# Kernel tuning notes

Hardware: AMD Instinct MI355X
Metric: run time of the kernel (lower is better)

Reference implementation:

```python
import jax, jax.numpy as jnp
import numpy as np
from jax.ops import segment_sum

N_NODES = 100000

def setup_inputs() -> dict:
    key = jax.random.key(0)
    k1, k2, k3 = jax.random.split(key, 3)
    x = jax.random.normal(k1, (N_NODES, 128), dtype=jnp.float32)
    edge_weight = jax.random.uniform(k2, (3200000,), dtype=jnp.float32)
    edge_index = jax.random.randint(k3, (2, 3200000), 0, N_NODES, dtype=jnp.int64)
    return {"x": x, "edge_weight": edge_weight, "edge_index": edge_index}

def reference(x, edge_weight, edge_index):
    # GCNConv with weight forced to identity (in==out channels, no bias):
    # lin(x) == x, so the op is gcn_norm + scatter-add aggregation.
    n = x.shape[0]
    # add self loops with fill value 1.0 (improved=False)
    loop_idx = jnp.arange(n, dtype=edge_index.dtype)
    row = jnp.concatenate([edge_index[0], loop_idx])
    col = jnp.concatenate([edge_index[1], loop_idx])
    ew = jnp.concatenate([edge_weight, jnp.ones((n,), dtype=edge_weight.dtype)])
    # symmetric normalization: deg computed at target (col)
    deg = segment_sum(ew, col, num_segments=n)
    dinv = jnp.where(deg > 0, jax.lax.rsqrt(deg), 0.0)
    norm = dinv[row] * ew * dinv[col]
    # message = norm * x[src]; aggregate (sum) at target
    msgs = x[row] * norm[:, None]          # [E+N, d]
    out = segment_sum(msgs, col, num_segments=n)  # [N, d]
    return out
```

## Files before the change

### kernel.cpp

```cpp
#include <hip/hip_runtime.h>
#include <hip/hip_fp16.h>
#include <math.h>

#define FEAT    128
#define PITCH   72
#define CH      6144
#define K_EDGES 12
#define MAXBINS 512

__global__ void zero_meta_kernel(float* __restrict__ deg, int* __restrict__ countg,
                                 int* __restrict__ cursor, int n, int nbins) {
    int i = blockIdx.x * blockDim.x + threadIdx.x;
    if (i < n) { deg[i] = 0.0f; countg[i] = 0; }
    if (i < nbins) cursor[i] = 0;
}

__global__ void conv_xs_kernel(const float* __restrict__ x,
                               const float* __restrict__ deg,
                               __half2* __restrict__ xs, int n4) {
    int i = blockIdx.x * blockDim.x + threadIdx.x;
    if (i >= n4) return;
    float s = rsqrtf(1.0f + deg[i >> 5]);
    float4 v = ((const float4*)x)[i];
    xs[2 * i]     = __floats2half2_rn(s * v.x, s * v.y);
    xs[2 * i + 1] = __floats2half2_rn(s * v.z, s * v.w);
}

__global__ __launch_bounds__(512) void p1_partition_kernel(
        const int* __restrict__ row,
        const int* __restrict__ col,
        const float* __restrict__ ew,
        int* __restrict__ bin_cursor,
        unsigned long long* __restrict__ binned,
        int E, int NBINS, int cap) {
    __shared__ unsigned long long stage[CH];
    __shared__ int hist[MAXBINS];
    __shared__ int lofs[MAXBINS];
    __shared__ int lcnt[MAXBINS];
    __shared__ int gbase[MAXBINS];
    __shared__ int scanbuf[MAXBINS];
    int tid = threadIdx.x;
    if (tid < MAXBINS) { hist[tid] = 0; lcnt[tid] = 0; }
    __syncthreads();

    int start = blockIdx.x * CH;
    int end   = start + CH; if (end > E) end = E;
    int total = end - start;

    unsigned long long ed[K_EDGES];
    int ebin[K_EDGES];
    #pragma unroll
    for (int k = 0; k < K_EDGES; k++) {
        int e = start + (k << 9) + tid;
        if (e < end) {
            int c = col[e];
            unsigned short wh = __half_as_ushort(__float2half_rn(ew[e]));
            ed[k] = ((unsigned long long)wh << 48)
                  | ((unsigned long long)((unsigned)row[e] & 0xFFFFFFu) << 24)
                  | (unsigned)(c & 0xFFFFFFu);
            ebin[k] = c >> 8;
            atomicAdd(&hist[ebin[k]], 1);
        } else {
            ebin[k] = -1;
        }
    }
    __syncthreads();

    int h = (tid < NBINS) ? hist[tid] : 0;
    scanbuf[tid] = h;
    __syncthreads();
    #pragma unroll
    for (int off = 1; off < MAXBINS; off <<= 1) {
        int t = (tid >= off) ? scanbuf[tid - off] : 0;
        __syncthreads();
        scanbuf[tid] += t;
        __syncthreads();
    }
    lofs[tid] = scanbuf[tid] - h;
    __syncthreads();

    #pragma unroll
    for (int k = 0; k < K_EDGES; k++) {
        if (ebin[k] >= 0) {
            int pos = lofs[ebin[k]] + atomicAdd(&lcnt[ebin[k]], 1);
            stage[pos] = ed[k];
        }
    }
    if (tid < NBINS)
        gbase[tid] = hist[tid] ? atomicAdd(&bin_cursor[tid], hist[tid]) : 0;
    __syncthreads();

    for (int i = tid; i < total; i += 512) {
        unsigned long long e = stage[i];
        int bin = (int)((e >> 8) & 0xFFFFu);
        int pos = gbase[bin] + (i - lofs[bin]);
        if (pos < cap) binned[(size_t)bin * cap + pos] = e;
    }
}

__global__ __launch_bounds__(256) void p2_build_kernel(
        const unsigned long long* __restrict__ binned,
        const int* __restrict__ bin_cursor,
        unsigned long long* __restrict__ bucket,
        float* __restrict__ deg,
        int* __restrict__ countg,
        int N, int cap) {
    __shared__ float degp[256];
    __shared__ int   cnt[256];
    int tid = threadIdx.x;
    degp[tid] = 0.0f;
    cnt[tid]  = 0;
    __syncthreads();

    int b = blockIdx.x >> 1, hf = blockIdx.x & 1;
    int nE = bin_cursor[b]; if (nE > cap) nE = cap;
    int half = nE >> 1;
    int lo = hf ? half : 0;
    int hi = hf ? nE : half;
    const unsigned long long* src = binned + (size_t)b * cap;
    int nodeBase = b << 8;

    for (int i = lo + tid; i < hi; i += 256) {
        unsigned long long p = src[i];
        int cl = (int)(p & 255u);
        int r  = (int)((p >> 24) & 0xFFFFFFu);
        float w = __half2float(__ushort_as_half((unsigned short)(p >> 48)));
        int slot = atomicAdd(&cnt[cl], 1);
        atomicAdd(&degp[cl], w);
        if (slot < PITCH) {
            int pos = hf ? (PITCH - 1 - slot) : slot;
            bucket[(size_t)(nodeBase + cl) * PITCH + pos] =
                ((unsigned long long)__float_as_uint(w) << 32) | (unsigned)r;
        }
    }
    __syncthreads();

    int node = nodeBase + tid;
    if (node < N) {
        int c2 = cnt[tid]; if (c2 > PITCH) c2 = PITCH;
        if (c2) atomicAdd(&countg[node], hf ? (c2 << 16) : c2);
        float d = degp[tid];
        if (d != 0.0f) atomicAdd(&deg[node], d);
    }
}

__global__ __launch_bounds__(256) void gather_xs_kernel(
        const __half2* __restrict__ xs,
        const float* __restrict__ deg,
        const int* __restrict__ countg,
        const unsigned long long* __restrict__ bucket,
        float* __restrict__ out, int n) {
    __shared__ unsigned long long eb[4][64];
    int wid  = threadIdx.x >> 6;
    int node = blockIdx.x * 4 + wid;
    int lane = threadIdx.x & 63;
    if (node >= n) return;

    float di = rsqrtf(1.0f + deg[node]);
    int c = countg[node];
    int cnt0 = c & 0xFFFF, cnt1 = (c >> 16) & 0xFFFF;
    int cnt = cnt0 + cnt1; if (cnt > PITCH) cnt = PITCH;

    const unsigned long long* b = bucket + (size_t)node * PITCH;
    int idx = (lane < cnt0) ? lane : (PITCH - 1 - (lane - cnt0));
    unsigned long long e0 = (lane < cnt) ? b[idx] : 0ULL;
    eb[wid][lane] = e0;

    unsigned xbase = ((unsigned)node << 6) | (unsigned)lane;
    float2 xv = __half22float2(xs[xbase]);
    float2 a0 = xv;
    float2 a1 = {0.f, 0.f}, a2 = {0.f, 0.f}, a3 = {0.f, 0.f};

    int m = cnt < 64 ? cnt : 64;
    int j = 0;
    for (; j + 8 <= m; j += 8) {
        unsigned long long p0 = eb[wid][j + 0];
        unsigned long long p1 = eb[wid][j + 1];
        unsigned long long p2 = eb[wid][j + 2];
        unsigned long long p3 = eb[wid][j + 3];
        unsigned long long p4 = eb[wid][j + 4];
        unsigned long long p5 = eb[wid][j + 5];
        unsigned long long p6 = eb[wid][j + 6];
        unsigned long long p7 = eb[wid][j + 7];
        unsigned r0 = (unsigned)p0, r1 = (unsigned)p1, r2 = (unsigned)p2, r3 = (unsigned)p3;
        unsigned r4 = (unsigned)p4, r5 = (unsigned)p5, r6 = (unsigned)p6, r7 = (unsigned)p7;
        float w0 = __uint_as_float((unsigned)(p0 >> 32));
        float w1 = __uint_as_float((unsigned)(p1 >> 32));
        float w2 = __uint_as_float((unsigned)(p2 >> 32));
        float w3 = __uint_as_float((unsigned)(p3 >> 32));
        float w4 = __uint_as_float((unsigned)(p4 >> 32));
        float w5 = __uint_as_float((unsigned)(p5 >> 32));
        float w6 = __uint_as_float((unsigned)(p6 >> 32));
        float w7 = __uint_as_float((unsigned)(p7 >> 32));
        float2 v0 = __half22float2(xs[(r0 << 6) | lane]);
        float2 v1 = __half22float2(xs[(r1 << 6) | lane]);
        float2 v2 = __half22float2(xs[(r2 << 6) | lane]);
        float2 v3 = __half22float2(xs[(r3 << 6) | lane]);
        float2 v4 = __half22float2(xs[(r4 << 6) | lane]);
        float2 v5 = __half22float2(xs[(r5 << 6) | lane]);
        float2 v6 = __half22float2(xs[(r6 << 6) | lane]);
        float2 v7 = __half22float2(xs[(r7 << 6) | lane]);
        a0.x = fmaf(w0, v0.x, a0.x);  a0.y = fmaf(w0, v0.y, a0.y);
        a1.x = fmaf(w1, v1.x, a1.x);  a1.y = fmaf(w1, v1.y, a1.y);
        a2.x = fmaf(w2, v2.x, a2.x);  a2.y = fmaf(w2, v2.y, a2.y);
        a3.x = fmaf(w3, v3.x, a3.x);  a3.y = fmaf(w3, v3.y, a3.y);
        a0.x = fmaf(w4, v4.x, a0.x);  a0.y = fmaf(w4, v4.y, a0.y);
        a1.x = fmaf(w5, v5.x, a1.x);  a1.y = fmaf(w5, v5.y, a1.y);
        a2.x = fmaf(w6, v6.x, a2.x);  a2.y = fmaf(w6, v6.y, a2.y);
        a3.x = fmaf(w7, v7.x, a3.x);  a3.y = fmaf(w7, v7.y, a3.y);
    }
    for (; j + 4 <= m; j += 4) {
        unsigned long long p0 = eb[wid][j + 0];
        unsigned long long p1 = eb[wid][j + 1];
        unsigned long long p2 = eb[wid][j + 2];
        unsigned long long p3 = eb[wid][j + 3];
        unsigned r0 = (unsigned)p0, r1 = (unsigned)p1, r2 = (unsigned)p2, r3 = (unsigned)p3;
        float w0 = __uint_as_float((unsigned)(p0 >> 32));
        float w1 = __uint_as_float((unsigned)(p1 >> 32));
        float w2 = __uint_as_float((unsigned)(p2 >> 32));
        float w3 = __uint_as_float((unsigned)(p3 >> 32));
        float2 v0 = __half22float2(xs[(r0 << 6) | lane]);
        float2 v1 = __half22float2(xs[(r1 << 6) | lane]);
        float2 v2 = __half22float2(xs[(r2 << 6) | lane]);
        float2 v3 = __half22float2(xs[(r3 << 6) | lane]);
        a0.x = fmaf(w0, v0.x, a0.x);  a0.y = fmaf(w0, v0.y, a0.y);
        a1.x = fmaf(w1, v1.x, a1.x);  a1.y = fmaf(w1, v1.y, a1.y);
        a2.x = fmaf(w2, v2.x, a2.x);  a2.y = fmaf(w2, v2.y, a2.y);
        a3.x = fmaf(w3, v3.x, a3.x);  a3.y = fmaf(w3, v3.y, a3.y);
    }
    for (; j < m; ++j) {
        unsigned long long p0 = eb[wid][j];
        unsigned r0 = (unsigned)p0;
        float w0 = __uint_as_float((unsigned)(p0 >> 32));
        float2 v0 = __half22float2(xs[(r0 << 6) | lane]);
        a0.x = fmaf(w0, v0.x, a0.x);  a0.y = fmaf(w0, v0.y, a0.y);
    }
    for (; j < cnt; ++j) {
        int jj = (j < cnt0) ? j : (PITCH - 1 - (j - cnt0));
        unsigned long long p0 = b[jj];
        unsigned r0 = (unsigned)p0;
        float w0 = __uint_as_float((unsigned)(p0 >> 32));
        float2 v0 = __half22float2(xs[(r0 << 6) | lane]);
        a0.x = fmaf(w0, v0.x, a0.x);  a0.y = fmaf(w0, v0.y, a0.y);
    }
    float2 r;
    r.x = di * ((a0.x + a1.x) + (a2.x + a3.x));
    r.y = di * ((a0.y + a1.y) + (a2.y + a3.y));
    ((float2*)(out + (size_t)node * FEAT))[lane] = r;
}


__global__ void init_packed_kernel(unsigned long long* __restrict__ packed, int n) {
    int i = blockIdx.x * blockDim.x + threadIdx.x;
    if (i < n) packed[i] = (1ULL << 32);
}

__global__ void passA_kernel(const int* __restrict__ row,
                             const int* __restrict__ col,
                             const float* __restrict__ ew,
                             unsigned long long* __restrict__ packed,
                             unsigned long long* __restrict__ bucket, int E) {
    int e = blockIdx.x * blockDim.x + threadIdx.x;
    if (e >= E) return;
    int c = col[e], r = row[e];
    float w = ew[e];
    unsigned long long v = (1ULL << 40)
        | (unsigned long long)((double)w * 4294967296.0);
    unsigned long long old = atomicAdd(&packed[c], v);
    unsigned int slot = (unsigned int)(old >> 40);
    if (slot < PITCH)
        bucket[(size_t)c * PITCH + slot] =
            ((unsigned long long)__float_as_uint(w) << 32) | (unsigned int)r;
}

__global__ void make_deg_count_kernel(const unsigned long long* __restrict__ packed,
                                      float* __restrict__ deg,
                                      int* __restrict__ countg, int n) {
    int i = blockIdx.x * blockDim.x + threadIdx.x;
    if (i < n) {
        unsigned long long p = packed[i];
        unsigned long long frac = p & ((1ULL << 40) - 1);
        float d = (float)((double)frac * (1.0 / 4294967296.0));
        deg[i] = d - 1.0f;
        int c = (int)(p >> 40); if (c > PITCH) c = PITCH;
        countg[i] = c;
    }
}


__global__ void init_deg_kernel(float* __restrict__ deg, int n) {
    int i = blockIdx.x * blockDim.x + threadIdx.x;
    if (i < n) deg[i] = 1.0f;
}
__global__ void deg_accum_kernel(const int* __restrict__ col,
                                 const float* __restrict__ ew,
                                 float* __restrict__ deg, int E) {
    int e = blockIdx.x * blockDim.x + threadIdx.x;
    if (e < E) atomicAdd(&deg[col[e]], ew[e]);
}
__global__ void make_dinv_kernel(const float* __restrict__ deg,
                                 float* __restrict__ dinv, int n) {
    int i = blockIdx.x * blockDim.x + threadIdx.x;
    if (i < n) {
        float d = deg[i];
        dinv[i] = d > 0.0f ? rsqrtf(d) : 0.0f;
    }
}
__global__ void init_out_kernel(const float* __restrict__ x,
                                const float* __restrict__ dinv,
                                float* __restrict__ out, int n) {
    int idx = blockIdx.x * blockDim.x + threadIdx.x;
    int i = idx >> 5, lane = idx & 31;
    if (i >= n) return;
    float s = dinv[i] * dinv[i];
    float4 v = ((const float4*)(x + (size_t)i * FEAT))[lane];
    float4 r;
    r.x = s * v.x; r.y = s * v.y; r.z = s * v.z; r.w = s * v.w;
    ((float4*)(out + (size_t)i * FEAT))[lane] = r;
}
__global__ void scatter_kernel(const float* __restrict__ x,
                               const float* __restrict__ ew,
                               const int* __restrict__ row,
                               const int* __restrict__ col,
                               const float* __restrict__ dinv,
                               float* __restrict__ out, int E) {
    long long idx = (long long)blockIdx.x * blockDim.x + threadIdx.x;
    int e = (int)(idx >> 5), lane = (int)(idx & 31);
    if (e >= E) return;
    int r = row[e], c = col[e];
    float nrm = dinv[r] * ew[e] * dinv[c];
    float4 v = ((const float4*)(x + (size_t)r * FEAT))[lane];
    float* o = out + (size_t)c * FEAT + lane * 4;
    atomicAdd(o + 0, nrm * v.x);
    atomicAdd(o + 1, nrm * v.y);
    atomicAdd(o + 2, nrm * v.z);
    atomicAdd(o + 3, nrm * v.w);
}


static inline size_t align256(size_t v) { return (v + 255) & ~(size_t)255; }

extern "C" void kernel_launch(void* const* d_in, const int* in_sizes, int n_in,
                              void* d_out, int out_size, void* d_ws, size_t ws_size,
                              hipStream_t stream) {
    const float* x  = (const float*)d_in[0];
    const float* ew = (const float*)d_in[1];
    const int*   ei = (const int*)d_in[2];

    const int N = in_sizes[0] / FEAT;
    const int E = in_sizes[1];
    const int* row = ei;
    const int* col = ei + E;

    float* out = (float*)d_out;
    const int B = 256;
    char* w = (char*)d_ws;

    const int NBINS = (N + 255) >> 8;
    const int avg   = (E + NBINS - 1) / NBINS;
    const int cap   = avg + 8 * (int)sqrt((double)avg) + 64;

    size_t sz_bucket = align256((size_t)N * PITCH * 8);
    size_t sz_deg    = align256((size_t)N * 4);
    size_t sz_count  = align256((size_t)N * 4);
    size_t sz_cursor = align256((size_t)NBINS * 4);
    size_t sz_binned = align256((size_t)NBINS * (size_t)cap * 8);
    size_t sz_xs     = align256((size_t)N * FEAT * 2);
    size_t sz_shared = sz_binned > sz_xs ? sz_binned : sz_xs;

    size_t need_fast2 = sz_bucket + sz_deg + sz_count + sz_cursor + sz_shared;
    size_t need_fast1 = align256((size_t)N * 8) + sz_deg + sz_count + sz_xs + sz_bucket;

    int nodes_per_block = B / 64;
    int gblocks = (N + nodes_per_block - 1) / nodes_per_block;
    int n4 = N * FEAT / 4;
    int zgrid = ((N > NBINS ? N : NBINS) + B - 1) / B;

    if (ws_size >= need_fast2 && NBINS <= MAXBINS && N < (1 << 24)) {
        unsigned long long* bucket = (unsigned long long*)w;  w += sz_bucket;
        float* deg    = (float*)w;                            w += sz_deg;
        int*   countg = (int*)w;                              w += sz_count;
        int*   cursor = (int*)w;                              w += sz_cursor;
        unsigned long long* binned = (unsigned long long*)w;
        __half2* xs = (__half2*)binned;

        zero_meta_kernel<<<zgrid, B, 0, stream>>>(deg, countg, cursor, N, NBINS);
        int p1b = (E + CH - 1) / CH;
        p1_partition_kernel<<<p1b, 512, 0, stream>>>(row, col, ew, cursor, binned,
                                                     E, NBINS, cap);
        p2_build_kernel<<<2 * NBINS, B, 0, stream>>>(binned, cursor, bucket,
                                                     deg, countg, N, cap);
        conv_xs_kernel<<<(n4 + B - 1) / B, B, 0, stream>>>(x, deg, xs, n4);
        gather_xs_kernel<<<gblocks, B, 0, stream>>>(xs, deg, countg, bucket, out, N);
    } else if (ws_size >= need_fast1 && N < (1 << 24)) {
        unsigned long long* packed = (unsigned long long*)w;  w += align256((size_t)N * 8);
        float*   deg    = (float*)w;                          w += sz_deg;
        int*     countg = (int*)w;                            w += sz_count;
        __half2* xs     = (__half2*)w;                        w += sz_xs;
        unsigned long long* bucket = (unsigned long long*)w;

        init_packed_kernel<<<(N + B - 1) / B, B, 0, stream>>>(packed, N);
        passA_kernel<<<(E + B - 1) / B, B, 0, stream>>>(row, col, ew, packed, bucket, E);
        make_deg_count_kernel<<<(N + B - 1) / B, B, 0, stream>>>(packed, deg, countg, N);
        conv_xs_kernel<<<(n4 + B - 1) / B, B, 0, stream>>>(x, deg, xs, n4);
        gather_xs_kernel<<<gblocks, B, 0, stream>>>(xs, deg, countg, bucket, out, N);
    } else {
        float* deg  = (float*)w;                  w += sz_deg;
        float* dinv = (float*)w;
        init_deg_kernel<<<(N + B - 1) / B, B, 0, stream>>>(deg, N);
        deg_accum_kernel<<<(E + B - 1) / B, B, 0, stream>>>(col, ew, deg, E);
        make_dinv_kernel<<<(N + B - 1) / B, B, 0, stream>>>(deg, dinv, N);
        long long it = (long long)N * 32;
        init_out_kernel<<<(int)((it + B - 1) / B), B, 0, stream>>>(x, dinv, out, N);
        long long st = (long long)E * 32;
        scatter_kernel<<<(int)((st + B - 1) / B), B, 0, stream>>>(x, ew, row, col, dinv, out, E);
    }
}
```

Before: 300.0 us.

## Build compact CSR per bin in shared memory instead of padded per-node buckets

The second partition pass now uses one 512-thread block per 256-node bin. Each block counts edges per node, computes a prefix sum, sorts the bin's edges into shared memory and writes a compact CSR segment at a base offset taken from a global atomic cursor. Degree and count are written directly, so the zero-meta kernel becomes a memset. This removes the padded PITCH-wide bucket array and the split-half reverse indexing, and the gather reads contiguous edge runs. In exchange it uses a large shared-memory stage, which limits occupancy, and caps per-node count at 255 and per-bin edges at STAGE_CAP.

```diff
diff --git a/kernel.cpp b/kernel.cpp
--- a/kernel.cpp
+++ b/kernel.cpp
@@ -2,18 +2,13 @@
 #include <hip/hip_fp16.h>
 #include <math.h>
 
-#define FEAT    128
-#define PITCH   72
-#define CH      6144
-#define K_EDGES 12
-#define MAXBINS 512
-
-__global__ void zero_meta_kernel(float* __restrict__ deg, int* __restrict__ countg,
-                                 int* __restrict__ cursor, int n, int nbins) {
-    int i = blockIdx.x * blockDim.x + threadIdx.x;
-    if (i < n) { deg[i] = 0.0f; countg[i] = 0; }
-    if (i < nbins) cursor[i] = 0;
-}
+#define FEAT      128
+#define PITCH     72
+#define CH        6144
+#define K_EDGES   12
+#define MAXBINS   512
+#define STAGE_CAP 9216
+#define K2        18
 
 __global__ void conv_xs_kernel(const float* __restrict__ x,
                                const float* __restrict__ deg,
@@ -98,49 +93,90 @@
     }
 }
 
-__global__ __launch_bounds__(256) void p2_build_kernel(
+__global__ __launch_bounds__(512) void p2_build_kernel(
         const unsigned long long* __restrict__ binned,
-        const int* __restrict__ bin_cursor,
-        unsigned long long* __restrict__ bucket,
+        int* __restrict__ bin_cursor,
+        unsigned long long* __restrict__ csr,
         float* __restrict__ deg,
         int* __restrict__ countg,
-        int N, int cap) {
-    __shared__ float degp[256];
-    __shared__ int   cnt[256];
+        int N, int NBINS, int cap) {
+    __shared__ unsigned long long stage[STAGE_CAP];
+    __shared__ float degf[256];
+    __shared__ int cnt[256];
+    __shared__ int pfx[256];
+    __shared__ int lcnt[256];
+    __shared__ int wsum[4];
+    __shared__ int binBase_s;
     int tid = threadIdx.x;
-    degp[tid] = 0.0f;
-    cnt[tid]  = 0;
-    __syncthreads();
-
-    int b = blockIdx.x >> 1, hf = blockIdx.x & 1;
+    if (tid < 256) { degf[tid] = 0.0f; cnt[tid] = 0; lcnt[tid] = 0; }
+    __syncthreads();
+
+    int b = blockIdx.x;
     int nE = bin_cursor[b]; if (nE > cap) nE = cap;
-    int half = nE >> 1;
-    int lo = hf ? half : 0;
-    int hi = hf ? nE : half;
     const unsigned long long* src = binned + (size_t)b * cap;
     int nodeBase = b << 8;
 
-    for (int i = lo + tid; i < hi; i += 256) {
-        unsigned long long p = src[i];
-        int cl = (int)(p & 255u);
-        int r  = (int)((p >> 24) & 0xFFFFFFu);
-        float w = __half2float(__ushort_as_half((unsigned short)(p >> 48)));
-        int slot = atomicAdd(&cnt[cl], 1);
-        atomicAdd(&degp[cl], w);
-        if (slot < PITCH) {
-            int pos = hf ? (PITCH - 1 - slot) : slot;
-            bucket[(size_t)(nodeBase + cl) * PITCH + pos] =
-                ((unsigned long long)__float_as_uint(w) << 32) | (unsigned)r;
-        }
-    }
-    __syncthreads();
-
-    int node = nodeBase + tid;
-    if (node < N) {
-        int c2 = cnt[tid]; if (c2 > PITCH) c2 = PITCH;
-        if (c2) atomicAdd(&countg[node], hf ? (c2 << 16) : c2);
-        float d = degp[tid];
-        if (d != 0.0f) atomicAdd(&deg[node], d);
+    unsigned long long ed[K2];
+    #pragma unroll
+    for (int k = 0; k < K2; k++) {
+        int i = tid + (k << 9);
+        if (i < nE) {
+            unsigned long long p = src[i];
+            int cl     = (int)(p & 255u);
+            unsigned r = (unsigned)((p >> 24) & 0xFFFFFFu);
+            float w = __half2float(__ushort_as_half((unsigned short)(p >> 48)));
+            atomicAdd(&cnt[cl], 1);
+            atomicAdd(&degf[cl], w);
+            ed[k] = ((unsigned long long)__float_as_uint(w) << 32)
+                  | ((unsigned)cl << 24) | r;
+        }
+    }
+    if (tid == 0) binBase_s = atomicAdd(&bin_cursor[NBINS], nE);
+    __syncthreads();
+
+    if (tid < 256) {
+        int w = tid >> 6, l = tid & 63;
+        int v = cnt[tid];
+        int inc = v;
+        #pragma unroll
+        for (int d = 1; d < 64; d <<= 1) {
+            int t = __shfl_up(inc, d);
+            if (l >= d) inc += t;
+        }
+        if (l == 63) wsum[w] = inc;
+        pfx[tid] = inc - v;
+    }
+    __syncthreads();
+    if (tid < 256) {
+        int w = tid >> 6;
+        int add = 0;
+        for (int q = 0; q < w; q++) add += wsum[q];
+        pfx[tid] += add;
+    }
+    __syncthreads();
+
+    #pragma unroll
+    for (int k = 0; k < K2; k++) {
+        int i = tid + (k << 9);
+        if (i < nE) {
+            unsigned long long p = ed[k];
+            int cl = (int)((p >> 24) & 255u);
+            int slot = atomicAdd(&lcnt[cl], 1);
+            stage[pfx[cl] + slot] = p & 0xFFFFFFFF00FFFFFFULL;
+        }
+    }
+    __syncthreads();
+
+    int binBase = binBase_s;
+    for (int i = tid; i < nE; i += 512)
+        csr[(size_t)binBase + i] = stage[i];
+    if (tid < 256) {
+        int node = nodeBase + tid;
+        if (node < N) {
+            deg[node] = degf[tid];
+            int c2 = cnt[tid]; if (c2 > 255) c2 = 255;
+            countg[node] = (int)((((unsigned)(binBase + pfx[tid])) << 8) | (unsigned)c2);
+        }
     }
 }
 
@@ -148,7 +184,7 @@
         const __half2* __restrict__ xs,
         const float* __restrict__ deg,
         const int* __restrict__ countg,
-        const unsigned long long* __restrict__ bucket,
+        const unsigned long long* __restrict__ csr,
         float* __restrict__ out, int n) {
     __shared__ unsigned long long eb[4][64];
     int wid  = threadIdx.x >> 6;
@@ -157,13 +193,11 @@
     if (node >= n) return;
 
     float di = rsqrtf(1.0f + deg[node]);
-    int c = countg[node];
-    int cnt0 = c & 0xFFFF, cnt1 = (c >> 16) & 0xFFFF;
-    int cnt = cnt0 + cnt1; if (cnt > PITCH) cnt = PITCH;
-
-    const unsigned long long* b = bucket + (size_t)node * PITCH;
-    int idx = (lane < cnt0) ? lane : (PITCH - 1 - (lane - cnt0));
-    unsigned long long e0 = (lane < cnt) ? b[idx] : 0ULL;
+    unsigned c = (unsigned)countg[node];
+    int cnt = (int)(c & 255u);
+    const unsigned long long* b = csr + (c >> 8);
+
+    unsigned long long e0 = (lane < cnt) ? b[lane] : 0ULL;
     eb[wid][lane] = e0;
 
     unsigned xbase = ((unsigned)node << 6) | (unsigned)lane;
@@ -236,8 +270,7 @@
         a0.x = fmaf(w0, v0.x, a0.x);  a0.y = fmaf(w0, v0.y, a0.y);
     }
     for (; j < cnt; ++j) {
-        int jj = (j < cnt0) ? j : (PITCH - 1 - (j - cnt0));
-        unsigned long long p0 = b[jj];
+        unsigned long long p0 = b[j];
         unsigned r0 = (unsigned)p0;
         float w0 = __uint_as_float((unsigned)(p0 >> 32));
         float2 v0 = __half22float2(xs[(r0 << 6) | lane]);
@@ -270,7 +303,7 @@
     unsigned int slot = (unsigned int)(old >> 40);
     if (slot < PITCH)
         bucket[(size_t)c * PITCH + slot] =
-            ((unsigned long long)__float_as_uint(w) << 32) | (unsigned int)r;
+            ((unsigned long long)__float_as_uint(w) << 32) | ((unsigned int)r & 0xFFFFFFu);
 }
 
 __global__ void make_deg_count_kernel(const unsigned long long* __restrict__ packed,
@@ -283,7 +316,7 @@
         float d = (float)((double)frac * (1.0 / 4294967296.0));
         deg[i] = d - 1.0f;
         int c = (int)(p >> 40); if (c > PITCH) c = PITCH;
-        countg[i] = c;
+        countg[i] = (int)((((unsigned)i * (unsigned)PITCH) << 8) | (unsigned)c);
     }
 }
 
@@ -358,41 +391,43 @@
 
     const int NBINS = (N + 255) >> 8;
     const int avg   = (E + NBINS - 1) / NBINS;
-    const int cap   = avg + 8 * (int)sqrt((double)avg) + 64;
-
+    int cap = avg + 8 * (int)sqrt((double)avg) + 64;
+    if (cap > STAGE_CAP) cap = STAGE_CAP;
+
+    size_t sz_csr    = align256((size_t)E * 8 + 256);
     size_t sz_bucket = align256((size_t)N * PITCH * 8);
     size_t sz_deg    = align256((size_t)N * 4);
     size_t sz_count  = align256((size_t)N * 4);
-    size_t sz_cursor = align256((size_t)NBINS * 4);
+    size_t sz_cursor = align256((size_t)(NBINS + 1) * 4);
     size_t sz_binned = align256((size_t)NBINS * (size_t)cap * 8);
     size_t sz_xs     = align256((size_t)N * FEAT * 2);
     size_t sz_shared = sz_binned > sz_xs ? sz_binned : sz_xs;
 
-    size_t need_fast2 = sz_bucket + sz_deg + sz_count + sz_cursor + sz_shared;
+    size_t need_fast2 = sz_csr + sz_deg + sz_count + sz_cursor + sz_shared;
     size_t need_fast1 = align256((size_t)N * 8) + sz_deg + sz_count + sz_xs + sz_bucket;
 
     int nodes_per_block = B / 64;
     int gblocks = (N + nodes_per_block - 1) / nodes_per_block;
     int n4 = N * FEAT / 4;
-    int zgrid = ((N > NBINS ? N : NBINS) + B - 1) / B;
-
-    if (ws_size >= need_fast2 && NBINS <= MAXBINS && N < (1 << 24)) {
-        unsigned long long* bucket = (unsigned long long*)w;  w += sz_bucket;
+
+    if (ws_size >= need_fast2 && NBINS <= MAXBINS && N < (1 << 24) && E < (1 << 24)) {
+        unsigned long long* csr = (unsigned long long*)w;     w += sz_csr;
         float* deg    = (float*)w;                            w += sz_deg;
         int*   countg = (int*)w;                              w += sz_count;
         int*   cursor = (int*)w;                              w += sz_cursor;
         unsigned long long* binned = (unsigned long long*)w;
         __half2* xs = (__half2*)binned;
 
-        zero_meta_kernel<<<zgrid, B, 0, stream>>>(deg, countg, cursor, N, NBINS);
+        hipMemsetAsync(cursor, 0, (size_t)(NBINS + 1) * 4, stream);
         int p1b = (E + CH - 1) / CH;
         p1_partition_kernel<<<p1b, 512, 0, stream>>>(row, col, ew, cursor, binned,
                                                      E, NBINS, cap);
-        p2_build_kernel<<<2 * NBINS, B, 0, stream>>>(binned, cursor, bucket,
-                                                     deg, countg, N, cap);
+        p2_build_kernel<<<NBINS, 512, 0, stream>>>(binned, cursor, csr,
+                                                   deg, countg, N, NBINS, cap);
         conv_xs_kernel<<<(n4 + B - 1) / B, B, 0, stream>>>(x, deg, xs, n4);
-        gather_xs_kernel<<<gblocks, B, 0, stream>>>(xs, deg, countg, bucket, out, N);
-    } else if (ws_size >= need_fast1 && N < (1 << 24)) {
+        gather_xs_kernel<<<gblocks, B, 0, stream>>>(xs, deg, countg, csr, out, N);
+    } else if (ws_size >= need_fast1 && N < (1 << 24) &&
+               (size_t)N * PITCH < (size_t)(1 << 24)) {
         unsigned long long* packed = (unsigned long long*)w;  w += align256((size_t)N * 8);
         float*   deg    = (float*)w;                          w += sz_deg;
         int*     countg = (int*)w;                            w += sz_count;
```

Result: no change. 295.0 us (-1.7%).
